# Kernel optimization log

Hardware: AMD Instinct MI355X
Metric: run time of the kernel (lower is better)

The kernel has to match this reference:

```python
import math
import jax, jax.numpy as jnp
import numpy as np

B, T, C, HS = 4, 4096, 2048, 128

def setup_inputs() -> dict:
    key = jax.random.key(0)
    k1, k2, k3, k4 = jax.random.split(key, 4)
    x = jax.random.normal(k1, (B, T, C), dtype=jnp.float32)
    # torch Linear init ~ U(-1/sqrt(in), 1/sqrt(in)); normal*0.02 is fine for a numeric baseline
    Wq = jax.random.normal(k2, (C, HS), dtype=jnp.float32) * 0.02
    Wk = jax.random.normal(k3, (C, HS), dtype=jnp.float32) * 0.02
    Wv = jax.random.normal(k4, (C, HS), dtype=jnp.float32) * 0.02
    return {"x": x, "Wq": Wq, "Wk": Wk, "Wv": Wv}

def reference(x, Wq, Wk, Wv):
    # Single-head causal self-attention (dropout in eval mode = identity).
    q = x @ Wq          # [B,T,HS]
    k = x @ Wk          # [B,T,HS]
    v = x @ Wv          # [B,T,HS]
    scale = 1.0 / math.sqrt(HS)
    att = jnp.einsum('bqd,bkd->bqk', q, k) * scale          # [B,T,T]
    causal = jnp.tril(jnp.ones((T, T), dtype=bool))          # [T,T]
    att = jnp.where(causal[None, :, :], att, -jnp.inf)
    att = jax.nn.softmax(att, axis=-1)
    y = jnp.einsum('bqk,bkd->bqd', att, v)                   # [B,T,HS]
    return y
```

## Files before the change

### kernel.cpp

```cpp
#include <hip/hip_runtime.h>
#include <hip/hip_bf16.h>


#define B_  4
#define T_  4096
#define C_  2048
#define HS_ 128

typedef unsigned short u16;
typedef __attribute__((ext_vector_type(8))) short short8;
typedef __attribute__((ext_vector_type(4))) float floatx4;

static __device__ __forceinline__ u16 f2bf(float x) {
  union { float f; unsigned u; } c; c.f = x;
  unsigned r = 0x7fffu + ((c.u >> 16) & 1u);
  return (u16)((c.u + r) >> 16);
}
static __device__ __forceinline__ u16 cvt_elem(float x) { return f2bf(x); }
static __device__ __forceinline__ u16 cvt_elem(u16 x) { return x; }

template <typename ST>
__global__ __launch_bounds__(256) void transpose_kernel(
    const ST* __restrict__ src, u16* __restrict__ dst, int R, int C) {
  __shared__ u16 tile[32][33];
  size_t moff = (size_t)blockIdx.z * (size_t)R * (size_t)C;
  src += moff; dst += moff;
  int c0 = blockIdx.x * 32, r0 = blockIdx.y * 32;
  int tx = threadIdx.x, ty = threadIdx.y;
#pragma unroll
  for (int i = 0; i < 4; ++i)
    tile[ty + 8 * i][tx] = cvt_elem(src[(size_t)(r0 + ty + 8 * i) * C + (c0 + tx)]);
  __syncthreads();
#pragma unroll
  for (int i = 0; i < 4; ++i)
    dst[(size_t)(c0 + ty + 8 * i) * R + (r0 + tx)] = tile[tx][ty + 8 * i];
}

#define GBM 128
#define GBK 64
#define LPAD 72

__global__ __launch_bounds__(256) void qkv_gemm_kernel(
    const float* __restrict__ X, const u16* __restrict__ WT3,
    u16* __restrict__ qkv) {
  __shared__ u16 Xs[GBM][LPAD];
  __shared__ u16 Ws[HS_][LPAD];
  int z = blockIdx.y;
  const u16* Wt = WT3 + (size_t)z * HS_ * C_;
  u16* outp = qkv + (size_t)z * ((size_t)B_ * T_ * HS_);
  int t = threadIdx.x;
  int wv = t >> 6, lane = t & 63;
  int l15 = lane & 15, hi = lane >> 4;
  int wm = (wv & 1) * 64, wn = (wv >> 1) * 64;
  size_t mbase = (size_t)blockIdx.x * GBM;

  floatx4 acc[4][4];
#pragma unroll
  for (int i = 0; i < 4; ++i)
#pragma unroll
    for (int j = 0; j < 4; ++j) acc[i][j] = (floatx4){0.f, 0.f, 0.f, 0.f};

  for (int kt = 0; kt < C_ / GBK; ++kt) {
#pragma unroll
    for (int i = 0; i < 4; ++i) {
      int id = i * 256 + t;
      int m = id >> 3, c = id & 7;
      const float* sp = &X[(mbase + m) * C_ + kt * GBK + c * 8];
      short8 v;
#pragma unroll
      for (int j = 0; j < 8; ++j) v[j] = (short)f2bf(sp[j]);
      *(short8*)&Xs[m][c * 8] = v;
    }
#pragma unroll
    for (int i = 0; i < 4; ++i) {
      int id = i * 256 + t;
      int n = id >> 3, c = id & 7;
      *(short8*)&Ws[n][c * 8] =
          *(const short8*)&Wt[(size_t)n * C_ + kt * GBK + c * 8];
    }
    __syncthreads();
#pragma unroll
    for (int ks = 0; ks < 2; ++ks) {
      short8 af[4], bf[4];
#pragma unroll
      for (int mt = 0; mt < 4; ++mt)
        af[mt] = *(const short8*)&Xs[wm + mt * 16 + l15][ks * 32 + hi * 8];
#pragma unroll
      for (int nt = 0; nt < 4; ++nt)
        bf[nt] = *(const short8*)&Ws[wn + nt * 16 + l15][ks * 32 + hi * 8];
#pragma unroll
      for (int mt = 0; mt < 4; ++mt)
#pragma unroll
        for (int nt = 0; nt < 4; ++nt)
          acc[mt][nt] = __builtin_amdgcn_mfma_f32_16x16x32_bf16(
              af[mt], bf[nt], acc[mt][nt], 0, 0, 0);
    }
    __syncthreads();
  }
#pragma unroll
  for (int mt = 0; mt < 4; ++mt)
#pragma unroll
    for (int nt = 0; nt < 4; ++nt)
#pragma unroll
      for (int r = 0; r < 4; ++r) {
        size_t row = mbase + wm + mt * 16 + hi * 4 + r;
        int col = wn + nt * 16 + l15;
        outp[row * HS_ + col] = f2bf(acc[mt][nt][r]);
      }
}

#define BQ 64
#define BKV 64
#define CHUNK 16

template <bool WRITE_PARTIAL>
static __device__ __forceinline__ void flash_body(
    const u16* __restrict__ q, const u16* __restrict__ k,
    const u16* __restrict__ vT, float* __restrict__ outO,
    float* __restrict__ Mp, float* __restrict__ Lp,
    int b, int qb, int kb0, int kb1, int slot) {
  __shared__ u16 Ks[BKV][136];
  __shared__ u16 Vs[HS_][72];
  __shared__ u16 Ps[BQ][72];
  int t = threadIdx.x;
  int wv = t >> 6, lane = t & 63, l15 = lane & 15, hi = lane >> 4;

  const float sc = 0.08838834764831845f * 1.4426950408889634f;

  short8 qf[4];
  {
    const u16* qrow = q + (size_t)(b * T_ + qb * BQ + wv * 16 + l15) * HS_;
#pragma unroll
    for (int ks = 0; ks < 4; ++ks)
      qf[ks] = *(const short8*)(qrow + ks * 32 + hi * 8);
  }

  floatx4 of[8];
#pragma unroll
  for (int dt = 0; dt < 8; ++dt) of[dt] = (floatx4){0.f, 0.f, 0.f, 0.f};
  float m_run[4], l_run[4];
#pragma unroll
  for (int r = 0; r < 4; ++r) { m_run[r] = -__builtin_inff(); l_run[r] = 0.f; }

  const u16* kbase = k + (size_t)b * T_ * HS_;
  const u16* vbase = vT + (size_t)b * HS_ * T_;

  for (int kb = kb0; kb <= kb1; ++kb) {
#pragma unroll
    for (int i = 0; i < 4; ++i) {
      int id = i * 256 + t;
      int n = id >> 4, c = id & 15;
      *(short8*)&Ks[n][c * 8] =
          *(const short8*)&kbase[(size_t)(kb * BKV + n) * HS_ + c * 8];
    }
#pragma unroll
    for (int i = 0; i < 4; ++i) {
      int id = i * 256 + t;
      int d = id >> 3, c = id & 7;
      *(short8*)&Vs[d][c * 8] =
          *(const short8*)&vbase[(size_t)d * T_ + kb * BKV + c * 8];
    }
    __syncthreads();

    floatx4 sf[4];
#pragma unroll
    for (int nt = 0; nt < 4; ++nt) {
      floatx4 s = (floatx4){0.f, 0.f, 0.f, 0.f};
#pragma unroll
      for (int ks = 0; ks < 4; ++ks) {
        short8 bfrag = *(const short8*)&Ks[nt * 16 + l15][ks * 32 + hi * 8];
        s = __builtin_amdgcn_mfma_f32_16x16x32_bf16(qf[ks], bfrag, s, 0, 0, 0);
      }
      sf[nt] = s;
    }

    float sv[4][4];
    if (kb == qb) {
#pragma unroll
      for (int nt = 0; nt < 4; ++nt) {
        int col = nt * 16 + l15;
#pragma unroll
        for (int r = 0; r < 4; ++r) {
          int row = wv * 16 + hi * 4 + r;
          sv[nt][r] = (col <= row) ? sf[nt][r] * sc : -__builtin_inff();
        }
      }
    } else {
#pragma unroll
      for (int nt = 0; nt < 4; ++nt)
#pragma unroll
        for (int r = 0; r < 4; ++r) sv[nt][r] = sf[nt][r] * sc;
    }

    float mt4[4], alpha[4];
#pragma unroll
    for (int r = 0; r < 4; ++r)
      mt4[r] = fmaxf(fmaxf(sv[0][r], sv[1][r]), fmaxf(sv[2][r], sv[3][r]));
#pragma unroll
    for (int off = 1; off < 16; off <<= 1)
#pragma unroll
      for (int r = 0; r < 4; ++r)
        mt4[r] = fmaxf(mt4[r], __shfl_xor(mt4[r], off));
#pragma unroll
    for (int r = 0; r < 4; ++r) {
      float mn = fmaxf(m_run[r], mt4[r]);
      alpha[r] = exp2f(m_run[r] - mn);
      m_run[r] = mn;
    }
    float pv[4][4], lt[4];
#pragma unroll
    for (int nt = 0; nt < 4; ++nt)
#pragma unroll
      for (int r = 0; r < 4; ++r) pv[nt][r] = exp2f(sv[nt][r] - m_run[r]);
#pragma unroll
    for (int r = 0; r < 4; ++r)
      lt[r] = (pv[0][r] + pv[1][r]) + (pv[2][r] + pv[3][r]);
#pragma unroll
    for (int off = 1; off < 16; off <<= 1)
#pragma unroll
      for (int r = 0; r < 4; ++r) lt[r] += __shfl_xor(lt[r], off);
#pragma unroll
    for (int r = 0; r < 4; ++r) l_run[r] = l_run[r] * alpha[r] + lt[r];
#pragma unroll
    for (int dt = 0; dt < 8; ++dt)
#pragma unroll
      for (int r = 0; r < 4; ++r) of[dt][r] *= alpha[r];

#pragma unroll
    for (int nt = 0; nt < 4; ++nt)
#pragma unroll
      for (int r = 0; r < 4; ++r)
        Ps[wv * 16 + hi * 4 + r][nt * 16 + l15] = f2bf(pv[nt][r]);
    __asm__ volatile("s_waitcnt lgkmcnt(0)" ::: "memory");

#pragma unroll
    for (int ks2 = 0; ks2 < 2; ++ks2) {
      short8 af = *(const short8*)&Ps[wv * 16 + l15][ks2 * 32 + hi * 8];
#pragma unroll
      for (int dt = 0; dt < 8; ++dt) {
        short8 bfrag = *(const short8*)&Vs[dt * 16 + l15][ks2 * 32 + hi * 8];
        of[dt] = __builtin_amdgcn_mfma_f32_16x16x32_bf16(af, bfrag, of[dt], 0, 0, 0);
      }
    }
    __syncthreads();
  }

  if (WRITE_PARTIAL) {
    float* Op = outO + (size_t)slot * (BQ * HS_);
#pragma unroll
    for (int dt = 0; dt < 8; ++dt)
#pragma unroll
      for (int r = 0; r < 4; ++r) {
        int row = wv * 16 + hi * 4 + r;
        Op[row * HS_ + dt * 16 + l15] = of[dt][r];
      }
    if (l15 == 0) {
#pragma unroll
      for (int r = 0; r < 4; ++r) {
        int row = wv * 16 + hi * 4 + r;
        Mp[slot * BQ + row] = m_run[r];
        Lp[slot * BQ + row] = l_run[r];
      }
    }
  } else {
    float rl[4];
#pragma unroll
    for (int r = 0; r < 4; ++r) rl[r] = 1.0f / l_run[r];
#pragma unroll
    for (int dt = 0; dt < 8; ++dt)
#pragma unroll
      for (int r = 0; r < 4; ++r) {
        size_t row = (size_t)(b * T_ + qb * BQ + wv * 16 + hi * 4 + r);
        outO[row * HS_ + dt * 16 + l15] = of[dt][r] * rl[r];
      }
  }
}

__global__ __launch_bounds__(256) void flash_partial_kernel(
    const u16* __restrict__ q, const u16* __restrict__ k,
    const u16* __restrict__ vT, float* __restrict__ Opart,
    float* __restrict__ Mpart, float* __restrict__ Lpart) {
  int qb = blockIdx.x, c = blockIdx.y, b = blockIdx.z;
  int kb0 = c * CHUNK;
  if (kb0 > qb) return;
  int kb1 = min(qb, kb0 + CHUNK - 1);
  int slot = (b * (T_ / BQ) + qb) * 4 + c;
  flash_body<true>(q, k, vT, Opart, Mpart, Lpart, b, qb, kb0, kb1, slot);
}

__global__ __launch_bounds__(256) void flash_attn_kernel(
    const u16* __restrict__ q, const u16* __restrict__ k,
    const u16* __restrict__ vT, float* __restrict__ out) {
  int qb = blockIdx.x, b = blockIdx.y;
  flash_body<false>(q, k, vT, out, nullptr, nullptr, b, qb, 0, qb, 0);
}

__global__ __launch_bounds__(256) void flash_merge_kernel(
    const float* __restrict__ Opart, const float* __restrict__ Mpart,
    const float* __restrict__ Lpart, float* __restrict__ out) {
  __shared__ float w[4][BQ];
  __shared__ float invL[BQ];
  int qb = blockIdx.x, b = blockIdx.y;
  int t = threadIdx.x;
  int nch = qb / CHUNK + 1;
  int slot0 = (b * (T_ / BQ) + qb) * 4;

  if (t < BQ) {
    float mv[4], mmax = -__builtin_inff();
    for (int c = 0; c < nch; ++c) {
      mv[c] = Mpart[(slot0 + c) * BQ + t];
      mmax = fmaxf(mmax, mv[c]);
    }
    float L = 0.f;
    for (int c = 0; c < nch; ++c) {
      float wc = exp2f(mv[c] - mmax);
      w[c][t] = wc;
      L += wc * Lpart[(slot0 + c) * BQ + t];
    }
    invL[t] = 1.0f / L;
  }
  __syncthreads();

  size_t obase = ((size_t)(b * T_) + (size_t)qb * BQ) * HS_;
#pragma unroll
  for (int j = 0; j < 32; ++j) {
    int e = j * 256 + t;
    int row = e >> 7;
    float acc = 0.f;
    for (int c = 0; c < nch; ++c)
      acc += w[c][row] * Opart[(size_t)(slot0 + c) * (BQ * HS_) + e];
    out[obase + e] = acc * invL[row];
  }
}

extern "C" void kernel_launch(void* const* d_in, const int* in_sizes, int n_in,
                              void* d_out, int out_size, void* d_ws, size_t ws_size,
                              hipStream_t stream) {
  const float* x  = (const float*)d_in[0];
  const float* Wq = (const float*)d_in[1];
  const float* Wk = (const float*)d_in[2];
  const float* Wv = (const float*)d_in[3];
  float* out = (float*)d_out;

  u16* ws = (u16*)d_ws;
  const size_t wtsz  = (size_t)HS_ * C_;
  const size_t qkvsz = (size_t)B_ * T_ * HS_;
  u16* WT = ws;
  u16* qv = WT + 3 * wtsz;
  u16* kv = qv + qkvsz;
  u16* vv = kv + qkvsz;
  u16* vT = vv + qkvsz;
  const size_t base_bytes = (3 * wtsz + 4 * qkvsz) * sizeof(u16);

  const int NSLOT = B_ * (T_ / BQ) * 4;
  float* Opart = (float*)((char*)d_ws + base_bytes);
  float* Mpart = Opart + (size_t)NSLOT * BQ * HS_;
  float* Lpart = Mpart + (size_t)NSLOT * BQ;
  const size_t split_bytes =
      base_bytes + ((size_t)NSLOT * BQ * HS_ + 2 * (size_t)NSLOT * BQ) * sizeof(float);

  dim3 tb(32, 8);
  transpose_kernel<float><<<dim3(HS_ / 32, C_ / 32, 1), tb, 0, stream>>>(Wq, WT + 0 * wtsz, C_, HS_);
  transpose_kernel<float><<<dim3(HS_ / 32, C_ / 32, 1), tb, 0, stream>>>(Wk, WT + 1 * wtsz, C_, HS_);
  transpose_kernel<float><<<dim3(HS_ / 32, C_ / 32, 1), tb, 0, stream>>>(Wv, WT + 2 * wtsz, C_, HS_);

  qkv_gemm_kernel<<<dim3((B_ * T_) / GBM, 3), 256, 0, stream>>>(x, WT, qv);

  transpose_kernel<u16><<<dim3(HS_ / 32, T_ / 32, B_), tb, 0, stream>>>(vv, vT, T_, HS_);

  if (ws_size >= split_bytes) {
    flash_partial_kernel<<<dim3(T_ / BQ, 4, B_), 256, 0, stream>>>(
        qv, kv, vT, Opart, Mpart, Lpart);
    flash_merge_kernel<<<dim3(T_ / BQ, B_), 256, 0, stream>>>(
        Opart, Mpart, Lpart, out);
  } else {
    flash_attn_kernel<<<dim3(T_ / BQ, B_), 256, 0, stream>>>(qv, kv, vT, out);
  }
}
```

Before: 353.1 us.

## Prefetch K/V into registers, fold row-sum into MFMA, lazily rescale softmax

The next K/V tile is loaded into registers while the current tile is computed, overlapping global loads with MFMA work. The softmax denominator now comes from an extra ones-row added to the V tile, so one more MFMA replaces the shuffle reduction. The running max and output rescale are skipped unless some row's max grows by more than 8 in log2 space. Launch bounds now request 3 blocks per SM. The extra prefetch registers and the ninth accumulator add register pressure, and the lazy rescale leaves exponentials up to 2^8 above the stored max before they are rounded to bf16.

```diff
diff --git a/kernel.cpp b/kernel.cpp
--- a/kernel.cpp
+++ b/kernel.cpp
@@ -120,7 +120,7 @@
     float* __restrict__ Mp, float* __restrict__ Lp,
     int b, int qb, int kb0, int kb1, int slot) {
   __shared__ u16 Ks[BKV][136];
-  __shared__ u16 Vs[HS_][72];
+  __shared__ u16 Vs[144][72];
   __shared__ u16 Ps[BQ][72];
   int t = threadIdx.x;
   int wv = t >> 6, lane = t & 63, l15 = lane & 15, hi = lane >> 4;
@@ -135,32 +135,54 @@
       qf[ks] = *(const short8*)(qrow + ks * 32 + hi * 8);
   }
 
-  floatx4 of[8];
-#pragma unroll
-  for (int dt = 0; dt < 8; ++dt) of[dt] = (floatx4){0.f, 0.f, 0.f, 0.f};
-  float m_run[4], l_run[4];
-#pragma unroll
-  for (int r = 0; r < 4; ++r) { m_run[r] = -__builtin_inff(); l_run[r] = 0.f; }
+  {
+    int r = 128 + (t >> 4), c0 = (t & 15) * 4;
+    const u16 one = 0x3F80;
+    Vs[r][c0] = one; Vs[r][c0 + 1] = one;
+    Vs[r][c0 + 2] = one; Vs[r][c0 + 3] = one;
+  }
+
+  floatx4 of[9];
+#pragma unroll
+  for (int dt = 0; dt < 9; ++dt) of[dt] = (floatx4){0.f, 0.f, 0.f, 0.f};
+  float m_run[4];
+#pragma unroll
+  for (int r = 0; r < 4; ++r) m_run[r] = -__builtin_inff();
 
   const u16* kbase = k + (size_t)b * T_ * HS_;
   const u16* vbase = vT + (size_t)b * HS_ * T_;
 
+  short8 kreg[4], vreg[4];
+#pragma unroll
+  for (int i = 0; i < 4; ++i) {
+    int id = i * 256 + t;
+    int n = id >> 4, ck = id & 15;
+    kreg[i] = *(const short8*)&kbase[(size_t)(kb0 * BKV + n) * HS_ + ck * 8];
+    int d = id >> 3, cv = id & 7;
+    vreg[i] = *(const short8*)&vbase[(size_t)d * T_ + kb0 * BKV + cv * 8];
+  }
+
   for (int kb = kb0; kb <= kb1; ++kb) {
 #pragma unroll
     for (int i = 0; i < 4; ++i) {
       int id = i * 256 + t;
-      int n = id >> 4, c = id & 15;
-      *(short8*)&Ks[n][c * 8] =
-          *(const short8*)&kbase[(size_t)(kb * BKV + n) * HS_ + c * 8];
-    }
-#pragma unroll
-    for (int i = 0; i < 4; ++i) {
-      int id = i * 256 + t;
-      int d = id >> 3, c = id & 7;
-      *(short8*)&Vs[d][c * 8] =
-          *(const short8*)&vbase[(size_t)d * T_ + kb * BKV + c * 8];
+      int n = id >> 4, ck = id & 15;
+      *(short8*)&Ks[n][ck * 8] = kreg[i];
+      int d = id >> 3, cv = id & 7;
+      *(short8*)&Vs[d][cv * 8] = vreg[i];
     }
     __syncthreads();
+
+    if (kb < kb1) {
+#pragma unroll
+      for (int i = 0; i < 4; ++i) {
+        int id = i * 256 + t;
+        int n = id >> 4, ck = id & 15;
+        kreg[i] = *(const short8*)&kbase[(size_t)((kb + 1) * BKV + n) * HS_ + ck * 8];
+        int d = id >> 3, cv = id & 7;
+        vreg[i] = *(const short8*)&vbase[(size_t)d * T_ + (kb + 1) * BKV + cv * 8];
+      }
+    }
 
     floatx4 sf[4];
 #pragma unroll
@@ -192,7 +214,7 @@
         for (int r = 0; r < 4; ++r) sv[nt][r] = sf[nt][r] * sc;
     }
 
-    float mt4[4], alpha[4];
+    float mt4[4];
 #pragma unroll
     for (int r = 0; r < 4; ++r)
       mt4[r] = fmaxf(fmaxf(sv[0][r], sv[1][r]), fmaxf(sv[2][r], sv[3][r]));
@@ -201,30 +223,29 @@
 #pragma unroll
       for (int r = 0; r < 4; ++r)
         mt4[r] = fmaxf(mt4[r], __shfl_xor(mt4[r], off));
-#pragma unroll
-    for (int r = 0; r < 4; ++r) {
-      float mn = fmaxf(m_run[r], mt4[r]);
-      alpha[r] = exp2f(m_run[r] - mn);
-      m_run[r] = mn;
-    }
-    float pv[4][4], lt[4];
+
+    bool need = false;
+#pragma unroll
+    for (int r = 0; r < 4; ++r) need = need || (mt4[r] > m_run[r] + 8.f);
+    if (__any(need)) {
+      float alpha[4];
+#pragma unroll
+      for (int r = 0; r < 4; ++r) {
+        float mn = fmaxf(m_run[r], mt4[r]);
+        alpha[r] = exp2f(m_run[r] - mn);
+        m_run[r] = mn;
+      }
+#pragma unroll
+      for (int dt = 0; dt < 9; ++dt)
+#pragma unroll
+        for (int r = 0; r < 4; ++r) of[dt][r] *= alpha[r];
+    }
+
+    float pv[4][4];
 #pragma unroll
     for (int nt = 0; nt < 4; ++nt)
 #pragma unroll
       for (int r = 0; r < 4; ++r) pv[nt][r] = exp2f(sv[nt][r] - m_run[r]);
-#pragma unroll
-    for (int r = 0; r < 4; ++r)
-      lt[r] = (pv[0][r] + pv[1][r]) + (pv[2][r] + pv[3][r]);
-#pragma unroll
-    for (int off = 1; off < 16; off <<= 1)
-#pragma unroll
-      for (int r = 0; r < 4; ++r) lt[r] += __shfl_xor(lt[r], off);
-#pragma unroll
-    for (int r = 0; r < 4; ++r) l_run[r] = l_run[r] * alpha[r] + lt[r];
-#pragma unroll
-    for (int dt = 0; dt < 8; ++dt)
-#pragma unroll
-      for (int r = 0; r < 4; ++r) of[dt][r] *= alpha[r];
 
 #pragma unroll
     for (int nt = 0; nt < 4; ++nt)
@@ -237,7 +258,7 @@
     for (int ks2 = 0; ks2 < 2; ++ks2) {
       short8 af = *(const short8*)&Ps[wv * 16 + l15][ks2 * 32 + hi * 8];
 #pragma unroll
-      for (int dt = 0; dt < 8; ++dt) {
+      for (int dt = 0; dt < 9; ++dt) {
         short8 bfrag = *(const short8*)&Vs[dt * 16 + l15][ks2 * 32 + hi * 8];
         of[dt] = __builtin_amdgcn_mfma_f32_16x16x32_bf16(af, bfrag, of[dt], 0, 0, 0);
       }
@@ -259,13 +280,13 @@
       for (int r = 0; r < 4; ++r) {
         int row = wv * 16 + hi * 4 + r;
         Mp[slot * BQ + row] = m_run[r];
-        Lp[slot * BQ + row] = l_run[r];
+        Lp[slot * BQ + row] = of[8][r];
       }
     }
   } else {
     float rl[4];
 #pragma unroll
-    for (int r = 0; r < 4; ++r) rl[r] = 1.0f / l_run[r];
+    for (int r = 0; r < 4; ++r) rl[r] = 1.0f / of[8][r];
 #pragma unroll
     for (int dt = 0; dt < 8; ++dt)
 #pragma unroll
@@ -276,7 +297,7 @@
   }
 }
 
-__global__ __launch_bounds__(256) void flash_partial_kernel(
+__global__ __launch_bounds__(256, 3) void flash_partial_kernel(
     const u16* __restrict__ q, const u16* __restrict__ k,
     const u16* __restrict__ vT, float* __restrict__ Opart,
     float* __restrict__ Mpart, float* __restrict__ Lpart) {
@@ -288,7 +309,7 @@
   flash_body<true>(q, k, vT, Opart, Mpart, Lpart, b, qb, kb0, kb1, slot);
 }
 
-__global__ __launch_bounds__(256) void flash_attn_kernel(
+__global__ __launch_bounds__(256, 3) void flash_attn_kernel(
     const u16* __restrict__ q, const u16* __restrict__ k,
     const u16* __restrict__ vT, float* __restrict__ out) {
   int qb = blockIdx.x, b = blockIdx.y;
```

Result: faster. 326.2 us (-7.6%).
